# Kernel optimization log

Measured on AMD Instinct MI355X. Metric: run time of the kernel, lower is better.

## Reference

```python
import jax, jax.numpy as jnp
import numpy as np


def _conv(x, w, b=None, stride=1, pad=0, dil=1):
    out = jax.lax.conv_general_dilated(
        x, w, (stride, stride), [(pad, pad), (pad, pad)],
        rhs_dilation=(dil, dil),
        dimension_numbers=('NCHW', 'OIHW', 'NCHW'))
    return out if b is None else out + b[None, :, None, None]


def _sobel_base(out_ch, in_ch, k=3):
    # Exactly mirrors SobelConv2d weight construction (4 directional kernels).
    w = np.zeros((out_ch, in_ch, k, k), np.float32)
    m = k // 2
    for idx in range(out_ch):
        if idx % 4 == 0:
            w[idx, :, 0, :] = -1; w[idx, :, 0, m] = -2
            w[idx, :, -1, :] = 1; w[idx, :, -1, m] = 2
        elif idx % 4 == 1:
            w[idx, :, :, 0] = -1; w[idx, :, m, 0] = -2
            w[idx, :, :, -1] = 1; w[idx, :, m, -1] = 2
        elif idx % 4 == 2:
            w[idx, :, 0, 0] = -2
            for i in range(m + 1):
                w[idx, :, m - i, i] = -1
                w[idx, :, k - 1 - i, m + i] = 1
            w[idx, :, -1, -1] = 2
        else:
            w[idx, :, -1, 0] = -2
            for i in range(m + 1):
                w[idx, :, m + i, i] = -1
                w[idx, :, i, m + i] = 1
            w[idx, :, 0, -1] = 2
    return w


def setup_inputs() -> dict:
    key = jax.random.key(0)
    ks = iter(jax.random.split(key, 40))
    def p(shape, s=0.05):
        return jax.random.normal(next(ks), shape, dtype=jnp.float32) * s
    C = 32  # out_ch == sobel_ch
    f32 = jnp.float32
    return dict(
        x=jax.random.normal(next(ks), (8, 1, 256, 256), dtype=f32),
        sobel_base=jnp.asarray(_sobel_base(C, 1)),
        sobel_factor=jnp.ones((C, 1, 1, 1), f32),
        sobel_bias=jnp.zeros((C,), f32),
        f4_w=p((C, C + 1, 3, 3)), f4_b=jnp.zeros((C,), f32),
        ec1_w=p((C, C, 3, 3)), ec1_b=jnp.zeros((C,), f32),
        ec2_w=p((C, C, 3, 3)), ec2_b=jnp.zeros((C,), f32),
        ec3_w=p((C, C, 3, 3)), ec3_b=jnp.zeros((C,), f32),
        gate_w=p((3, 3 * C, 1, 1)), gate_b=jnp.zeros((3,), f32),
        ca1_w=p((C // 16, C, 1, 1)),  # ChannelAttention fc1 (ratio=16), no bias
        ca2_w=p((C, C // 16, 1, 1)),  # fc2, no bias
        sa_w=p((1, 2, 7, 7)),         # SpatialAttention conv, no bias
        p1_w=p((C, C, 1, 1)), p1_b=jnp.zeros((C,), f32),
        f1_w=p((C, C, 3, 3)), f1_b=jnp.zeros((C,), f32),
        p2_w=p((C, 2 * C, 1, 1)), p2_b=jnp.zeros((C,), f32),
        f2_w=p((C, C, 3, 3)), f2_b=jnp.zeros((C,), f32),
        p3_w=p((C, 2 * C, 1, 1)), p3_b=jnp.zeros((C,), f32),
        f3_w=p((C, C, 3, 3)), f3_b=jnp.zeros((C,), f32),
    )


def reference(x, sobel_base, sobel_factor, sobel_bias, f4_w, f4_b,
              ec1_w, ec1_b, ec2_w, ec2_b, ec3_w, ec3_b, gate_w, gate_b,
              ca1_w, ca2_w, sa_w,
              p1_w, p1_b, f1_w, f1_b, p2_w, p2_b, f2_w, f2_b,
              p3_w, p3_b, f3_w, f3_b):
    lrelu = lambda t: jax.nn.leaky_relu(t, 0.01)
    relu = jax.nn.relu
    # Sobel edge extraction (fixed directional kernels scaled by learned factor)
    out0 = _conv(x, sobel_base * sobel_factor, sobel_bias, pad=1)     # [B,32,H,W]
    out1 = jnp.concatenate([x, out0], axis=1)                          # [B,33,H,W]
    out1 = lrelu(_conv(out1, f4_w, f4_b, pad=1))                       # [B,32,H,W]
    # AdaptiveEdgeConnector: multi-dilation convs + softmax gating
    ex = relu(_conv(out1, ec1_w, ec1_b, pad=1))
    ey = relu(_conv(out1, ec2_w, ec2_b, pad=2, dil=2))
    ez = relu(_conv(out1, ec3_w, ec3_b, pad=3, dil=3))
    gates = jax.nn.softmax(_conv(jnp.concatenate([ex, ey, ez], axis=1), gate_w, gate_b), axis=1)
    enh = gates[:, 0:1] * ex + gates[:, 1:2] * ey + gates[:, 2:3] * ez
    # CBAM: channel attention
    avg = jnp.mean(enh, axis=(2, 3), keepdims=True)
    mx = jnp.max(enh, axis=(2, 3), keepdims=True)
    ca = jax.nn.sigmoid(_conv(relu(_conv(avg, ca1_w)), ca2_w)
                        + _conv(relu(_conv(mx, ca1_w)), ca2_w))
    f = ca * enh
    # CBAM: spatial attention
    sa_in = jnp.concatenate([jnp.mean(f, axis=1, keepdims=True),
                             jnp.max(f, axis=1, keepdims=True)], axis=1)
    sa = jax.nn.sigmoid(_conv(sa_in, sa_w, pad=3))
    edge = sa * f
    # Residual merge + cascaded dense conv stages
    out0 = lrelu(out1 + edge)
    t = lrelu(_conv(out0, p1_w, p1_b))
    t = lrelu(_conv(t, f1_w, f1_b, pad=1))
    o1 = jnp.concatenate([out0, t], axis=1)                            # [B,64,H,W]
    t = lrelu(_conv(o1, p2_w, p2_b))
    t = lrelu(_conv(t, f2_w, f2_b, pad=1))
    o2 = jnp.concatenate([out0, t], axis=1)
    t = lrelu(_conv(o2, p3_w, p3_b))
    t = lrelu(_conv(t, f3_w, f3_b, pad=1))
    return jnp.concatenate([out0, t], axis=1)                          # [B,64,H,W]
```

## Files before the change

kernel.cpp:

```cpp
#include <hip/hip_runtime.h>
#include <math.h>

typedef unsigned short u16;
typedef short short8 __attribute__((ext_vector_type(8)));
typedef float f32x4 __attribute__((ext_vector_type(4)));
typedef unsigned short ushort4v __attribute__((ext_vector_type(4)));

#define Hh 256
#define Ww 256
#define Bb 8
#define PW 262
#define PAD 3
#define HPW (Hh * PW)

__device__ __forceinline__ float bf2f(u16 v) {
    unsigned u = ((unsigned)v) << 16;
    union { unsigned u; float f; } c; c.u = u; return c.f;
}
__device__ __forceinline__ u16 f2bf(float f) {
    union { float f; unsigned u; } c; c.f = f;
    unsigned lsb = (c.u >> 16) & 1u;
    c.u += 0x7fffu + lsb;
    return (u16)(c.u >> 16);
}
__device__ __forceinline__ float sigm(float v) { return 1.f / (1.f + expf(-v)); }

template<int ACT, bool F32OUT, bool FUSEP>
__global__ __launch_bounds__(256) void convs_k(
    const u16* __restrict__ in, const u16* __restrict__ apack,
    const float* __restrict__ bias, void* __restrict__ outp,
    const u16* __restrict__ o0buf, const u16* __restrict__ pw,
    const float* __restrict__ pb, u16* __restrict__ pout)
{
    __shared__ u16 rows[4][4352];
    const int tid = threadIdx.x, lane = tid & 63, wv = tid >> 6;
    const int b = blockIdx.x & 7;
    const int rest = blockIdx.x >> 3;
    const int hpair = rest >> 1, half = rest & 1;
    const int h0 = hpair * 2;
    const int pl = wv * 32 + (lane & 15);
    const int icg = lane >> 4;

    for (int idx = tid; idx < 4 * 536; idx += 256) {
        int rr = idx / 536, q = idx % 536;
        int r = h0 - 1 + rr;
        short8 v = (short8){0, 0, 0, 0, 0, 0, 0, 0};
        if ((unsigned)r < 256u)
            v = *(const short8*)(in + ((size_t)b * HPW + (size_t)r * PW + PAD + half * 128 - 3) * 32
                                 + (size_t)q * 8);
        *(short8*)(&rows[rr][q * 8]) = v;
    }
    __syncthreads();

    f32x4 acc[2][2][2];
    #pragma unroll
    for (int r2 = 0; r2 < 2; ++r2)
        #pragma unroll
        for (int mf = 0; mf < 2; ++mf)
            #pragma unroll
            for (int nf = 0; nf < 2; ++nf)
                acc[r2][mf][nf] = (f32x4){0.f, 0.f, 0.f, 0.f};

    #pragma unroll
    for (int tap = 0; tap < 9; ++tap) {
        const int kh = tap / 3 - 1, kw = tap % 3 - 1;
        short8 a0 = *(const short8*)(apack + ((size_t)(tap * 2 + 0) * 64 + lane) * 8);
        short8 a1 = *(const short8*)(apack + ((size_t)(tap * 2 + 1) * 64 + lane) * 8);
        #pragma unroll
        for (int r2 = 0; r2 < 2; ++r2) {
            const int ri = 1 + r2 + kh;
            #pragma unroll
            for (int nf = 0; nf < 2; ++nf) {
                short8 bf = *(const short8*)(&rows[ri][(pl + nf * 16 + kw + 3) * 32 + icg * 8]);
                acc[r2][0][nf] = __builtin_amdgcn_mfma_f32_16x16x32_bf16(a0, bf, acc[r2][0][nf], 0, 0, 0);
                acc[r2][1][nf] = __builtin_amdgcn_mfma_f32_16x16x32_bf16(a1, bf, acc[r2][1][nf], 0, 0, 0);
            }
        }
    }
    const int nl = half * 128 + pl;
    f32x4 bi[2];
    bi[0] = *(const f32x4*)(bias + icg * 4);
    bi[1] = *(const f32x4*)(bias + 16 + icg * 4);

    if (FUSEP) {
        u16* tile = &rows[0][0];
        __syncthreads();
        #pragma unroll
        for (int r2 = 0; r2 < 2; ++r2)
            #pragma unroll
            for (int mf = 0; mf < 2; ++mf) {
                const int cob = mf * 16 + icg * 4;
                #pragma unroll
                for (int nf = 0; nf < 2; ++nf) {
                    ushort4v o;
                    #pragma unroll
                    for (int i = 0; i < 4; ++i) {
                        float v = acc[r2][mf][nf][i] + bi[mf][i];
                        v = (v > 0.f) ? v : 0.01f * v;
                        o[i] = f2bf(v);
                    }
                    *(ushort4v*)(tile + ((size_t)(r2 * 128 + pl + nf * 16)) * 32 + cob) = o;
                }
            }
        __syncthreads();
        #pragma unroll
        for (int r2 = 0; r2 < 2; ++r2) {
            const int h = h0 + r2;
            f32x4 acc2[2][2];
            #pragma unroll
            for (int mf = 0; mf < 2; ++mf)
                #pragma unroll
                for (int nf = 0; nf < 2; ++nf)
                    acc2[mf][nf] = (f32x4){0.f, 0.f, 0.f, 0.f};
            #pragma unroll
            for (int s = 0; s < 2; ++s) {
                short8 pa0 = *(const short8*)(pw + (size_t)(s * 2 + 0) * 512 + lane * 8);
                short8 pa1 = *(const short8*)(pw + (size_t)(s * 2 + 1) * 512 + lane * 8);
                #pragma unroll
                for (int nf = 0; nf < 2; ++nf) {
                    const int px = pl + nf * 16;
                    short8 bf;
                    if (s == 0)
                        bf = *(const short8*)(o0buf + ((size_t)b * HPW + (size_t)h * PW + PAD + half * 128 + px) * 32 + icg * 8);
                    else
                        bf = *(const short8*)(tile + ((size_t)(r2 * 128 + px)) * 32 + icg * 8);
                    acc2[0][nf] = __builtin_amdgcn_mfma_f32_16x16x32_bf16(pa0, bf, acc2[0][nf], 0, 0, 0);
                    acc2[1][nf] = __builtin_amdgcn_mfma_f32_16x16x32_bf16(pa1, bf, acc2[1][nf], 0, 0, 0);
                }
            }
            const size_t orow = ((size_t)b * HPW + (size_t)h * PW + PAD) * 32;
            #pragma unroll
            for (int mf = 0; mf < 2; ++mf) {
                const int cob = mf * 16 + icg * 4;
                f32x4 pbi = *(const f32x4*)(pb + cob);
                #pragma unroll
                for (int nf = 0; nf < 2; ++nf) {
                    ushort4v o;
                    #pragma unroll
                    for (int i = 0; i < 4; ++i) {
                        float v = acc2[mf][nf][i] + pbi[i];
                        v = (v > 0.f) ? v : 0.01f * v;
                        o[i] = f2bf(v);
                    }
                    *(ushort4v*)(pout + orow + (size_t)(nl + nf * 16) * 32 + cob) = o;
                }
            }
        }
        if (tid < 24) {
            int r2 = tid / 12, rem = tid % 12;
            int col3 = rem >> 2, chunk = rem & 3;
            int col = half ? (256 + PAD + col3) : col3;
            u16* pz = pout + ((size_t)b * HPW + (size_t)(h0 + r2) * PW + col) * 32 + chunk * 8;
            *(short8*)pz = (short8){0, 0, 0, 0, 0, 0, 0, 0};
        }
    } else if (F32OUT) {
        #pragma unroll
        for (int r2 = 0; r2 < 2; ++r2) {
            float* dp = (float*)outp + ((size_t)b * 64 + 32) * 65536 + (size_t)(h0 + r2) * 256;
            #pragma unroll
            for (int mf = 0; mf < 2; ++mf) {
                const int cob = mf * 16 + icg * 4;
                #pragma unroll
                for (int nf = 0; nf < 2; ++nf) {
                    const int w = nl + nf * 16;
                    #pragma unroll
                    for (int i = 0; i < 4; ++i) {
                        float v = acc[r2][mf][nf][i] + bi[mf][i];
                        if (ACT == 1) v = fmaxf(v, 0.f);
                        if (ACT == 2) v = (v > 0.f) ? v : 0.01f * v;
                        dp[(size_t)(cob + i) * 65536 + w] = v;
                    }
                }
            }
        }
    } else {
        u16* out = (u16*)outp;
        #pragma unroll
        for (int r2 = 0; r2 < 2; ++r2) {
            const size_t orow = ((size_t)b * HPW + (size_t)(h0 + r2) * PW + PAD) * 32;
            #pragma unroll
            for (int mf = 0; mf < 2; ++mf) {
                const int cob = mf * 16 + icg * 4;
                #pragma unroll
                for (int nf = 0; nf < 2; ++nf) {
                    ushort4v o;
                    #pragma unroll
                    for (int i = 0; i < 4; ++i) {
                        float v = acc[r2][mf][nf][i] + bi[mf][i];
                        if (ACT == 1) v = fmaxf(v, 0.f);
                        if (ACT == 2) v = (v > 0.f) ? v : 0.01f * v;
                        o[i] = f2bf(v);
                    }
                    *(ushort4v*)(out + orow + (size_t)(nl + nf * 16) * 32 + cob) = o;
                }
            }
        }
    }
}

__global__ __launch_bounds__(256) void ecfuse_k(
    const u16* __restrict__ in, const u16* __restrict__ apack,
    const float* __restrict__ b1, const float* __restrict__ b2,
    const float* __restrict__ b3, const float* __restrict__ gw_,
    const float* __restrict__ gb_, u16* __restrict__ enh)
{
    __shared__ u16 rows[2][3][4288];
    __shared__ float gw[288];
    __shared__ float gb[3];
    __shared__ float bs[96];
    int tid = threadIdx.x;
    for (int i = tid; i < 288; i += 256) gw[i] = gw_[i];
    if (tid < 3) gb[tid] = gb_[tid];
    if (tid < 32) bs[tid] = b1[tid];
    else if (tid < 64) bs[tid] = b2[tid - 32];
    else if (tid < 96) bs[tid] = b3[tid - 64];

    const int lane = tid & 63, wv = tid >> 6;
    const int b = blockIdx.x & 7;
    const int rest = blockIdx.x >> 3;
    const int h = rest >> 1, half = rest & 1;
    const int pl = wv * 32 + (lane & 15);
    const int icg = lane >> 4;
    const u16* src_base = in + ((size_t)b * HPW + PAD + half * 128 - 3) * 32;

    for (int idx = tid; idx < 1608; idx += 256) {
        int rr = idx / 536, q = idx % 536;
        int r = h + (rr - 1);
        short8 v = (short8){0, 0, 0, 0, 0, 0, 0, 0};
        if ((unsigned)r < 256u)
            v = *(const short8*)(src_base + (size_t)r * PW * 32 + (size_t)q * 8);
        *(short8*)(&rows[0][rr][q * 8]) = v;
    }
    __syncthreads();

    f32x4 acc[3][2][2];
    #pragma unroll
    for (int cv = 0; cv < 3; ++cv)
        #pragma unroll
        for (int mf = 0; mf < 2; ++mf)
            #pragma unroll
            for (int nf = 0; nf < 2; ++nf)
                acc[cv][mf][nf] = (f32x4){0.f, 0.f, 0.f, 0.f};

    #pragma unroll
    for (int cv = 0; cv < 3; ++cv) {
        const int dil = cv + 1;
        const int nb = cv & 1;
        short8 stg0, stg1, stg2, stg3, stg4, stg5;
        if (cv < 2) {
            const int dn = cv + 2;
            #pragma unroll
            for (int k = 0; k < 6; ++k) {
                int idx = tid + k * 256;
                int rr = idx / 536, q = idx % 536;
                int r = h + (rr - 1) * dn;
                short8 v = (short8){0, 0, 0, 0, 0, 0, 0, 0};
                if ((unsigned)r < 256u)
                    v = *(const short8*)(src_base + (size_t)r * PW * 32 + (size_t)q * 8);
                if (k == 0) stg0 = v; else if (k == 1) stg1 = v;
                else if (k == 2) stg2 = v; else if (k == 3) stg3 = v;
                else if (k == 4) stg4 = v; else stg5 = v;
            }
        }
        const u16* ap = apack + (size_t)(cv * 9 * 2) * 512;
        #pragma unroll
        for (int tap = 0; tap < 9; ++tap) {
            const int kh = tap / 3 - 1, kw = tap % 3 - 1;
            const int ri = 1 + kh;
            short8 a0 = *(const short8*)(ap + (size_t)(tap * 2 + 0) * 512 + lane * 8);
            short8 a1 = *(const short8*)(ap + (size_t)(tap * 2 + 1) * 512 + lane * 8);
            #pragma unroll
            for (int nf = 0; nf < 2; ++nf) {
                short8 bf = *(const short8*)(&rows[nb][ri][(pl + nf * 16 + kw * dil + 3) * 32 + icg * 8]);
                acc[cv][0][nf] = __builtin_amdgcn_mfma_f32_16x16x32_bf16(a0, bf, acc[cv][0][nf], 0, 0, 0);
                acc[cv][1][nf] = __builtin_amdgcn_mfma_f32_16x16x32_bf16(a1, bf, acc[cv][1][nf], 0, 0, 0);
            }
        }
        if (cv < 2) {
            const int dn = cv + 2;
            #pragma unroll
            for (int k = 0; k < 6; ++k) {
                int idx = tid + k * 256;
                int rr = idx / 536, q = idx % 536;
                short8 v = (k == 0) ? stg0 : (k == 1) ? stg1 : (k == 2) ? stg2
                         : (k == 3) ? stg3 : (k == 4) ? stg4 : stg5;
                *(short8*)(&rows[1 - nb][rr][q * 8]) = v;
            }
            if (tid < 72) {
                int idx = tid + 1536;
                int rr = idx / 536, q = idx % 536;
                int r = h + (rr - 1) * dn;
                short8 v = (short8){0, 0, 0, 0, 0, 0, 0, 0};
                if ((unsigned)r < 256u)
                    v = *(const short8*)(src_base + (size_t)r * PW * 32 + (size_t)q * 8);
                *(short8*)(&rows[1 - nb][rr][q * 8]) = v;
            }
            __syncthreads();
        }
    }
    const int nl = half * 128 + pl;
    const size_t orow = ((size_t)b * HPW + (size_t)h * PW + PAD) * 32;
    #pragma unroll
    for (int nf = 0; nf < 2; ++nf) {
        float e[3][2][4];
        float g0 = 0.f, g1 = 0.f, g2 = 0.f;
        #pragma unroll
        for (int cv = 0; cv < 3; ++cv)
            #pragma unroll
            for (int mf = 0; mf < 2; ++mf) {
                const int cob = mf * 16 + icg * 4;
                #pragma unroll
                for (int i = 0; i < 4; ++i) {
                    float v = fmaxf(acc[cv][mf][nf][i] + bs[cv * 32 + cob + i], 0.f);
                    e[cv][mf][i] = v;
                    const int c = cv * 32 + cob + i;
                    g0 = fmaf(gw[c], v, g0);
                    g1 = fmaf(gw[96 + c], v, g1);
                    g2 = fmaf(gw[192 + c], v, g2);
                }
            }
        g0 += __shfl_xor(g0, 16); g0 += __shfl_xor(g0, 32);
        g1 += __shfl_xor(g1, 16); g1 += __shfl_xor(g1, 32);
        g2 += __shfl_xor(g2, 16); g2 += __shfl_xor(g2, 32);
        g0 += gb[0]; g1 += gb[1]; g2 += gb[2];
        float m = fmaxf(g0, fmaxf(g1, g2));
        float e0 = expf(g0 - m), e1 = expf(g1 - m), e2 = expf(g2 - m);
        float inv = 1.f / (e0 + e1 + e2);
        e0 *= inv; e1 *= inv; e2 *= inv;
        #pragma unroll
        for (int mf = 0; mf < 2; ++mf) {
            const int cob = mf * 16 + icg * 4;
            ushort4v o;
            #pragma unroll
            for (int i = 0; i < 4; ++i)
                o[i] = f2bf(e0 * e[0][mf][i] + e1 * e[1][mf][i] + e2 * e[2][mf][i]);
            *(ushort4v*)(enh + orow + (size_t)(nl + nf * 16) * 32 + cob) = o;
        }
    }
}

__global__ void prepack_k(
    const float* __restrict__ f4w, const float* __restrict__ e1w,
    const float* __restrict__ e2w, const float* __restrict__ e3w,
    const float* __restrict__ f1w, const float* __restrict__ f2w,
    const float* __restrict__ f3w, const float* __restrict__ p1w,
    const float* __restrict__ p2w, const float* __restrict__ p3w,
    u16* __restrict__ apack)
{
    int gid = blockIdx.x * 256 + threadIdx.x;
    if (gid >= 77 * 1024) return;
    const int offs[11] = {0, 18, 27, 36, 45, 54, 63, 72, 73, 75, 77};
    int step = gid >> 10, r = gid & 1023;
    int layer = 0;
    while (step >= offs[layer + 1]) layer++;
    int s = step - offs[layer];
    int mf = r >> 9, l = (r >> 3) & 63, j = r & 7;
    int co = mf * 16 + (l & 15);
    int ICB = (layer == 0 || layer == 8 || layer == 9) ? 2 : 1;
    int tap = s / ICB, icb = s % ICB;
    int icl = icb * 32 + (l >> 4) * 8 + j;
    float v = 0.f;
    if (layer == 0)      { if (icl < 33) v = f4w[(co * 33 + icl) * 9 + tap]; }
    else if (layer == 1) v = e1w[(co * 32 + icl) * 9 + tap];
    else if (layer == 2) v = e2w[(co * 32 + icl) * 9 + tap];
    else if (layer == 3) v = e3w[(co * 32 + icl) * 9 + tap];
    else if (layer == 4) v = f1w[(co * 32 + icl) * 9 + tap];
    else if (layer == 5) v = f2w[(co * 32 + icl) * 9 + tap];
    else if (layer == 6) v = f3w[(co * 32 + icl) * 9 + tap];
    else if (layer == 7) v = p1w[co * 32 + icl];
    else if (layer == 8) v = p2w[co * 64 + icl];
    else                 v = p3w[co * 64 + icl];
    apack[gid] = f2bf(v);
}

__global__ __launch_bounds__(256) void prep5_k(
    const float* __restrict__ f4w, const float* __restrict__ f4b,
    const float* __restrict__ sbase, const float* __restrict__ sfac,
    const float* __restrict__ sbias,
    float* __restrict__ w5, float* __restrict__ be)
{
    __shared__ float sF[32 * 33 * 9];
    __shared__ float sS[288];
    __shared__ float sBias[32];
    int t = threadIdx.x;
    for (int i = t; i < 32 * 33 * 9; i += 256) sF[i] = f4w[i];
    for (int i = t; i < 288; i += 256) sS[i] = sbase[i] * sfac[i / 9];
    if (t < 32) sBias[t] = sbias[t];
    __syncthreads();

    for (int idx = t; idx < 800; idx += 256) {
        int co = idx / 25, tap = idx % 25, kh = tap / 5, kw = tap % 5;
        float s = 0.f;
        if (kh >= 1 && kh <= 3 && kw >= 1 && kw <= 3)
            s = sF[(co * 33 + 0) * 9 + (kh - 1) * 3 + (kw - 1)];
        for (int sc = 0; sc < 32; ++sc) {
            #pragma unroll
            for (int a = 0; a < 3; ++a)
                #pragma unroll
                for (int bq = 0; bq < 3; ++bq) {
                    int p = kh - a, q = kw - bq;
                    if (p >= 0 && p < 3 && q >= 0 && q < 3)
                        s = fmaf(sF[(co * 33 + 1 + sc) * 9 + a * 3 + bq],
                                 sS[sc * 9 + p * 3 + q], s);
                }
        }
        w5[idx] = s;
    }
    for (int co = t; co < 32; co += 256) {
        float s = f4b[co];
        for (int sc = 0; sc < 32; ++sc) {
            float wsum = 0.f;
            #pragma unroll
            for (int k = 0; k < 9; ++k) wsum += sF[(co * 33 + 1 + sc) * 9 + k];
            s = fmaf(sBias[sc], wsum, s);
        }
        be[co] = s;
    }
}

__global__ __launch_bounds__(256) void conv5_k(
    const float* __restrict__ x, const float* __restrict__ w5,
    const float* __restrict__ be, u16* __restrict__ out1)
{
    __shared__ float sw[800];
    __shared__ float sb[32];
    int tid = threadIdx.x;
    for (int i = tid; i < 800; i += 256) sw[i] = w5[i];
    if (tid < 32) sb[tid] = be[tid];
    __syncthreads();
    int b = blockIdx.x & 7, h = blockIdx.x >> 3, w = tid;
    const float* xp = x + (size_t)b * 65536;
    float xv[25];
    #pragma unroll
    for (int i = 0; i < 5; ++i) {
        int r = h + i - 2;
        #pragma unroll
        for (int j = 0; j < 5; ++j) {
            int c = w + j - 2;
            xv[i * 5 + j] = ((unsigned)r < 256u && (unsigned)c < 256u)
                            ? xp[r * 256 + c] : 0.f;
        }
    }
    u16* dst = out1 + ((size_t)b * HPW + (size_t)h * PW + PAD + w) * 32;
    #pragma unroll
    for (int cb = 0; cb < 4; ++cb) {
        short8 o;
        #pragma unroll
        for (int j = 0; j < 8; ++j) {
            int co = cb * 8 + j;
            float s = sb[co];
            #pragma unroll
            for (int t2 = 0; t2 < 25; ++t2) s = fmaf(sw[co * 25 + t2], xv[t2], s);
            s = (s > 0.f) ? s : 0.01f * s;
            o[j] = (short)f2bf(s);
        }
        *(short8*)(dst + cb * 8) = o;
    }
    if (tid < 24) {
        int col6 = tid >> 2, chunk = tid & 3;
        int col = (col6 < 3) ? col6 : (256 + PAD + col6 - 3);
        u16* pz = out1 + ((size_t)b * HPW + (size_t)h * PW + col) * 32 + chunk * 8;
        *(short8*)pz = (short8){0, 0, 0, 0, 0, 0, 0, 0};
    }
}

__global__ __launch_bounds__(256) void ringfix_k(
    const float* __restrict__ x, const float* __restrict__ f4w,
    const float* __restrict__ f4b, const float* __restrict__ sbase,
    const float* __restrict__ sfac, const float* __restrict__ sbias,
    u16* __restrict__ out1)
{
    __shared__ float sW[288];
    __shared__ float sB[32];
    __shared__ float sF[32 * 33 * 9];
    __shared__ float sO[66][2][32];
    int tid = threadIdx.x;
    for (int i = tid; i < 288; i += 256) sW[i] = sbase[i] * sfac[i / 9];
    if (tid < 32) sB[tid] = sbias[tid];
    for (int i = tid; i < 32 * 33 * 9; i += 256) sF[i] = f4w[i];
    __syncthreads();

    int blk = blockIdx.x;
    int b = blk & 7, rest = blk >> 3;
    int e = rest >> 2, seg = rest & 3;
    const float* xp = x + (size_t)b * 65536;

    for (int i = tid; i < 66 * 2 * 32; i += 256) {
        int sc = i & 31, rr2 = i >> 5;
        int d = rr2 & 1, ul = rr2 >> 1;
        int ug = seg * 64 - 1 + ul;
        float v = 0.f;
        if ((unsigned)ug < 256u) {
            int h, w;
            if (e == 0)      { h = d;        w = ug; }
            else if (e == 1) { h = 255 - d;  w = ug; }
            else if (e == 2) { h = ug;       w = d; }
            else             { h = ug;       w = 255 - d; }
            float s = sB[sc];
            for (int p = 0; p < 3; ++p)
                for (int q = 0; q < 3; ++q) {
                    int rr = h + p - 1, cc = w + q - 1;
                    if ((unsigned)rr < 256u && (unsigned)cc < 256u)
                        s = fmaf(sW[sc * 9 + p * 3 + q], xp[rr * 256 + cc], s);
                }
            v = s;
        }
        sO[ul][d][sc] = v;
    }
    __syncthreads();

    int pi = tid & 63, cog = tid >> 6;
    int up = seg * 64 + pi;
    int h, w;
    if (e == 0)      { h = 0;   w = up; }
    else if (e == 1) { h = 255; w = up; }
    else if (e == 2) { h = up;  w = 0; }
    else             { h = up;  w = 255; }
    short8 ov;
    for (int cj = 0; cj < 8; ++cj) {
        int co = cog * 8 + cj;
        float acc = f4b[co];
        for (int a = 0; a < 3; ++a)
            for (int bb = 0; bb < 3; ++bb) {
                int hh = h + a - 1, ww = w + bb - 1;
                if ((unsigned)hh < 256u && (unsigned)ww < 256u)
                    acc = fmaf(sF[(co * 33) * 9 + a * 3 + bb], xp[hh * 256 + ww], acc);
                int d, ug;
                if (e == 0)      { d = hh;        ug = ww; }
                else if (e == 1) { d = 255 - hh;  ug = ww; }
                else if (e == 2) { d = ww;        ug = hh; }
                else             { d = 255 - ww;  ug = hh; }
                if (d >= 0 && d < 2 && (unsigned)ug < 256u) {
                    int ul = ug - (seg * 64 - 1);
                    for (int sc = 0; sc < 32; ++sc)
                        acc = fmaf(sF[(co * 33 + 1 + sc) * 9 + a * 3 + bb], sO[ul][d][sc], acc);
                }
            }
        acc = (acc > 0.f) ? acc : 0.01f * acc;
        ov[cj] = (short)f2bf(acc);
    }
    u16* dst = out1 + ((size_t)b * HPW + (size_t)h * PW + PAD + w) * 32 + cog * 8;
    *(short8*)dst = ov;
}

__global__ __launch_bounds__(256) void ca_part_k(
    const u16* __restrict__ enh, float* __restrict__ part)
{
    int blk = blockIdx.x, b = blk & 7, sl = blk >> 3;
    int tid = threadIdx.x, lane = tid & 63, wv = tid >> 6;
    float s[32], m[32];
    #pragma unroll
    for (int c = 0; c < 32; ++c) { s[c] = 0.f; m[c] = -1e30f; }
    for (int k = 0; k < 8; ++k) {
        int px = sl * 2048 + k * 256 + tid;
        int h = px >> 8, w = px & 255;
        size_t off = ((size_t)b * HPW + (size_t)h * PW + PAD + w) * 32;
        #pragma unroll
        for (int cb = 0; cb < 4; ++cb) {
            short8 v = *(const short8*)(enh + off + cb * 8);
            #pragma unroll
            for (int j = 0; j < 8; ++j) {
                float f = bf2f((u16)v[j]);
                s[cb * 8 + j] += f;
                m[cb * 8 + j] = fmaxf(m[cb * 8 + j], f);
            }
        }
    }
    #pragma unroll
    for (int c = 0; c < 32; ++c)
        #pragma unroll
        for (int o = 32; o; o >>= 1) {
            s[c] += __shfl_down(s[c], o);
            m[c] = fmaxf(m[c], __shfl_down(m[c], o));
        }
    __shared__ float ls[4][32], lm[4][32];
    if (lane == 0)
        for (int c = 0; c < 32; ++c) { ls[wv][c] = s[c]; lm[wv][c] = m[c]; }
    __syncthreads();
    if (tid < 32) {
        float ts = 0.f, tm = -1e30f;
        for (int w2 = 0; w2 < 4; ++w2) { ts += ls[w2][tid]; tm = fmaxf(tm, lm[w2][tid]); }
        int bs = b * 32 + sl;
        part[(size_t)(bs * 2 + 0) * 32 + tid] = ts;
        part[(size_t)(bs * 2 + 1) * 32 + tid] = tm;
    }
}

__global__ void ca_final_k(const float* __restrict__ part,
                           const float* __restrict__ w1, const float* __restrict__ w2,
                           float* __restrict__ ca)
{
    int t = threadIdx.x, b = t >> 5, c = t & 31;
    float s = 0.f, m = -1e30f;
    for (int sl = 0; sl < 32; ++sl) {
        int bs = b * 32 + sl;
        s += part[(size_t)(bs * 2 + 0) * 32 + c];
        m = fmaxf(m, part[(size_t)(bs * 2 + 1) * 32 + c]);
    }
    __shared__ float av[8][32], mx[8][32];
    av[b][c] = s * (1.f / 65536.f);
    mx[b][c] = m;
    __syncthreads();
    float sa0 = 0.f, sm0 = 0.f, sa1 = 0.f, sm1 = 0.f;
    for (int k = 0; k < 32; ++k) {
        float wa = w1[k], wb = w1[32 + k];
        sa0 = fmaf(wa, av[b][k], sa0); sm0 = fmaf(wa, mx[b][k], sm0);
        sa1 = fmaf(wb, av[b][k], sa1); sm1 = fmaf(wb, mx[b][k], sm1);
    }
    float h0 = fmaxf(sa0, 0.f) + fmaxf(sm0, 0.f);
    float h1 = fmaxf(sa1, 0.f) + fmaxf(sm1, 0.f);
    ca[t] = sigm(w2[c * 2 + 0] * h0 + w2[c * 2 + 1] * h1);
}

__global__ __launch_bounds__(256) void samap_k(
    const u16* __restrict__ enh, const float* __restrict__ ca,
    float* __restrict__ smap)
{
    __shared__ float sca[256];
    int tid = threadIdx.x;
    sca[tid] = ca[tid];
    __syncthreads();
    int b = blockIdx.x & 7;
    int r = (blockIdx.x >> 3) * 256 + tid;
    if (r >= 262 * 262) return;
    int ph = r / 262, pw = r % 262;
    float mean = 0.f, mxv = 0.f;
    if (ph >= 3 && ph < 259 && pw >= 3 && pw < 259) {
        int h = ph - 3, w = pw - 3;
        size_t off = ((size_t)b * HPW + (size_t)h * PW + PAD + w) * 32;
        float s = 0.f, m = -1e30f;
        #pragma unroll
        for (int cb = 0; cb < 4; ++cb) {
            short8 v = *(const short8*)(enh + off + cb * 8);
            #pragma unroll
            for (int j = 0; j < 8; ++j) {
                float f = bf2f((u16)v[j]) * sca[b * 32 + cb * 8 + j];
                s += f; m = fmaxf(m, f);
            }
        }
        mean = s * (1.f / 32.f); mxv = m;
    }
    smap[((size_t)b * 262 * 262 + (size_t)ph * 262 + pw) * 2 + 0] = mean;
    smap[((size_t)b * 262 * 262 + (size_t)ph * 262 + pw) * 2 + 1] = mxv;
}

__global__ __launch_bounds__(256) void merge_k(
    const float* __restrict__ smap, const float* __restrict__ saw,
    const float* __restrict__ ca, const u16* __restrict__ out1,
    const u16* __restrict__ enh, u16* __restrict__ o0,
    float* __restrict__ dout,
    const u16* __restrict__ ap1, const float* __restrict__ p1b,
    u16* __restrict__ p1out)
{
    __shared__ float sw[98];
    __shared__ float sca[256];
    __shared__ u16 tile[256 * 32];
    int tid = threadIdx.x;
    for (int i = tid; i < 98; i += 256) sw[i] = saw[i];
    sca[tid] = ca[tid];
    __syncthreads();
    int b = blockIdx.x & 7;
    int h = blockIdx.x >> 3;
    int w = tid;
    const float* sp = smap + (size_t)b * 262 * 262 * 2;
    float acc = 0.f;
    #pragma unroll
    for (int kh = 0; kh < 7; ++kh)
        #pragma unroll
        for (int kw = 0; kw < 7; ++kw) {
            const float* q = sp + ((size_t)(h + kh) * 262 + (w + kw)) * 2;
            acc = fmaf(q[0], sw[kh * 7 + kw], acc);
            acc = fmaf(q[1], sw[49 + kh * 7 + kw], acc);
        }
    float sa = sigm(acc);
    size_t off = ((size_t)b * HPW + (size_t)h * PW + PAD + w) * 32;
    float* dp = dout + (size_t)b * 64 * 65536 + (size_t)h * 256 + w;
    #pragma unroll
    for (int cb = 0; cb < 4; ++cb) {
        short8 ve = *(const short8*)(enh + off + cb * 8);
        short8 vo = *(const short8*)(out1 + off + cb * 8);
        short8 o;
        #pragma unroll
        for (int j = 0; j < 8; ++j) {
            float f = sca[b * 32 + cb * 8 + j] * bf2f((u16)ve[j]);
            float v = bf2f((u16)vo[j]) + sa * f;
            v = (v > 0.f) ? v : 0.01f * v;
            o[j] = (short)f2bf(v);
            dp[(size_t)(cb * 8 + j) * 65536] = v;
        }
        *(short8*)(o0 + off + cb * 8) = o;
        *(short8*)(&tile[w * 32 + cb * 8]) = o;
    }
    __syncthreads();
    const int lane = tid & 63, wv = tid >> 6;
    const int icg = lane >> 4, l15 = lane & 15;
    f32x4 acc1[2][4];
    #pragma unroll
    for (int mf = 0; mf < 2; ++mf)
        #pragma unroll
        for (int nf = 0; nf < 4; ++nf)
            acc1[mf][nf] = (f32x4){0.f, 0.f, 0.f, 0.f};
    short8 pa0 = *(const short8*)(ap1 + (size_t)0 * 512 + lane * 8);
    short8 pa1 = *(const short8*)(ap1 + (size_t)1 * 512 + lane * 8);
    #pragma unroll
    for (int nf = 0; nf < 4; ++nf) {
        short8 bf = *(const short8*)(&tile[(wv * 64 + l15 + nf * 16) * 32 + icg * 8]);
        acc1[0][nf] = __builtin_amdgcn_mfma_f32_16x16x32_bf16(pa0, bf, acc1[0][nf], 0, 0, 0);
        acc1[1][nf] = __builtin_amdgcn_mfma_f32_16x16x32_bf16(pa1, bf, acc1[1][nf], 0, 0, 0);
    }
    const size_t orow = ((size_t)b * HPW + (size_t)h * PW + PAD) * 32;
    #pragma unroll
    for (int mf = 0; mf < 2; ++mf) {
        const int cob = mf * 16 + icg * 4;
        f32x4 pbi = *(const f32x4*)(p1b + cob);
        #pragma unroll
        for (int nf = 0; nf < 4; ++nf) {
            const int px = wv * 64 + l15 + nf * 16;
            ushort4v o;
            #pragma unroll
            for (int i = 0; i < 4; ++i) {
                float v = acc1[mf][nf][i] + pbi[i];
                v = (v > 0.f) ? v : 0.01f * v;
                o[i] = f2bf(v);
            }
            *(ushort4v*)(p1out + orow + (size_t)px * 32 + cob) = o;
        }
    }
}

extern "C" void kernel_launch(void* const* d_in, const int* in_sizes, int n_in,
                              void* d_out, int out_size, void* d_ws, size_t ws_size,
                              hipStream_t stream)
{
    (void)in_sizes; (void)n_in; (void)out_size; (void)ws_size;
    const float* x        = (const float*)d_in[0];
    const float* sob_base = (const float*)d_in[1];
    const float* sob_fac  = (const float*)d_in[2];
    const float* sob_bias = (const float*)d_in[3];
    const float* f4_w = (const float*)d_in[4];   const float* f4_b = (const float*)d_in[5];
    const float* ec1_w = (const float*)d_in[6];  const float* ec1_b = (const float*)d_in[7];
    const float* ec2_w = (const float*)d_in[8];  const float* ec2_b = (const float*)d_in[9];
    const float* ec3_w = (const float*)d_in[10]; const float* ec3_b = (const float*)d_in[11];
    const float* gate_w = (const float*)d_in[12]; const float* gate_b = (const float*)d_in[13];
    const float* ca1_w = (const float*)d_in[14]; const float* ca2_w = (const float*)d_in[15];
    const float* sa_w  = (const float*)d_in[16];
    const float* p1_w = (const float*)d_in[17]; const float* p1_b = (const float*)d_in[18];
    const float* f1_w = (const float*)d_in[19]; const float* f1_b = (const float*)d_in[20];
    const float* p2_w = (const float*)d_in[21]; const float* p2_b = (const float*)d_in[22];
    const float* f2_w = (const float*)d_in[23]; const float* f2_b = (const float*)d_in[24];
    const float* p3_w = (const float*)d_in[25]; const float* p3_b = (const float*)d_in[26];
    const float* f3_w = (const float*)d_in[27]; const float* f3_b = (const float*)d_in[28];

    const size_t PB32 = (size_t)Bb * HPW * 32 * 2;
    char* ws = (char*)d_ws;
    u16* Q    = (u16*)(ws);
    u16* O0   = (u16*)(ws + PB32);
    u16* T    = (u16*)(ws + 2 * PB32);
    u16* ENH  = (u16*)(ws + 3 * PB32);
    u16* AP   = (u16*)(ws + 4 * PB32);
    float* W5   = (float*)(ws + 4 * PB32 + 77 * 1024 * 2);
    float* BE   = W5 + 800;
    float* PART = BE + 32;
    float* CA   = PART + 8 * 32 * 2 * 32;

    char* doutc = (char*)d_out;
    float* SMAP = (float*)(doutc + (134217728 - (size_t)Bb * 262 * 262 * 2 * 4));
    float* dout = (float*)d_out;

    dim3 blk(256);

    prepack_k<<<308, blk, 0, stream>>>(f4_w, ec1_w, ec2_w, ec3_w, f1_w, f2_w, f3_w,
                                       p1_w, p2_w, p3_w, AP);
    prep5_k<<<1, blk, 0, stream>>>(f4_w, f4_b, sob_base, sob_fac, sob_bias, W5, BE);
    conv5_k<<<2048, blk, 0, stream>>>(x, W5, BE, Q);
    ringfix_k<<<128, blk, 0, stream>>>(x, f4_w, f4_b, sob_base, sob_fac, sob_bias, Q);
    ecfuse_k<<<4096, blk, 0, stream>>>(Q, AP + 18 * 1024, ec1_b, ec2_b, ec3_b,
                                       gate_w, gate_b, ENH);
    ca_part_k<<<256, blk, 0, stream>>>(ENH, PART);
    ca_final_k<<<1, blk, 0, stream>>>(PART, ca1_w, ca2_w, CA);
    samap_k<<<2152, blk, 0, stream>>>(ENH, CA, SMAP);
    merge_k<<<2048, blk, 0, stream>>>(SMAP, sa_w, CA, Q, ENH, O0, dout,
                                      AP + 72 * 1024, p1_b, Q);
    convs_k<2, false, true ><<<2048, blk, 0, stream>>>(Q, AP + 45 * 1024, f1_b, nullptr,
                                                       O0, AP + 73 * 1024, p2_b, T);
    convs_k<2, false, true ><<<2048, blk, 0, stream>>>(T, AP + 54 * 1024, f2_b, nullptr,
                                                       O0, AP + 75 * 1024, p3_b, Q);
    convs_k<2, true, false><<<2048, blk, 0, stream>>>(Q, AP + 63 * 1024, f3_b, dout,
                                                      nullptr, nullptr, nullptr, nullptr);
}
```

Before: 389.7 us.

## Compute two output rows per block in fused dilated edge conv kernel

The fused three-dilation edge conv kernel now processes two adjacent output rows per block instead of one. The centre rows are loaded once and shared across both rows and all dilations, and only the dilation-specific halo rows are reloaded. This halves the grid and cuts redundant global and LDS row loads and weight fragment loads per output. In exchange it doubles accumulator registers and adds an extra barrier per dilation stage, which may lower occupancy.

```diff
diff --git a/kernel.cpp b/kernel.cpp
--- a/kernel.cpp
+++ b/kernel.cpp
@@ -204,7 +204,8 @@
     const float* __restrict__ b3, const float* __restrict__ gw_,
     const float* __restrict__ gb_, u16* __restrict__ enh)
 {
-    __shared__ u16 rows[2][3][4288];
+    __shared__ u16 crow[2][4288];
+    __shared__ u16 halo[4][4288];
     __shared__ float gw[288];
     __shared__ float gb[3];
     __shared__ float bs[96];
@@ -218,123 +219,142 @@
     const int lane = tid & 63, wv = tid >> 6;
     const int b = blockIdx.x & 7;
     const int rest = blockIdx.x >> 3;
-    const int h = rest >> 1, half = rest & 1;
+    const int hpair = rest >> 1, half = rest & 1;
+    const int h = hpair * 2;
     const int pl = wv * 32 + (lane & 15);
     const int icg = lane >> 4;
     const u16* src_base = in + ((size_t)b * HPW + PAD + half * 128 - 3) * 32;
 
-    for (int idx = tid; idx < 1608; idx += 256) {
+    for (int idx = tid; idx < 4 * 536; idx += 256) {
         int rr = idx / 536, q = idx % 536;
-        int r = h + (rr - 1);
+        int r = h - 1 + rr;
         short8 v = (short8){0, 0, 0, 0, 0, 0, 0, 0};
         if ((unsigned)r < 256u)
             v = *(const short8*)(src_base + (size_t)r * PW * 32 + (size_t)q * 8);
-        *(short8*)(&rows[0][rr][q * 8]) = v;
-    }
-    __syncthreads();
-
-    f32x4 acc[3][2][2];
+        u16* dst = (rr == 1) ? &crow[0][q * 8] : (rr == 2) ? &crow[1][q * 8]
+                 : (rr == 0) ? &halo[0][q * 8] : &halo[3][q * 8];
+        *(short8*)dst = v;
+    }
+    __syncthreads();
+
+    f32x4 acc[3][2][2][2];
     #pragma unroll
     for (int cv = 0; cv < 3; ++cv)
         #pragma unroll
-        for (int mf = 0; mf < 2; ++mf)
-            #pragma unroll
-            for (int nf = 0; nf < 2; ++nf)
-                acc[cv][mf][nf] = (f32x4){0.f, 0.f, 0.f, 0.f};
+        for (int r2 = 0; r2 < 2; ++r2)
+            #pragma unroll
+            for (int mf = 0; mf < 2; ++mf)
+                #pragma unroll
+                for (int nf = 0; nf < 2; ++nf)
+                    acc[cv][r2][mf][nf] = (f32x4){0.f, 0.f, 0.f, 0.f};
 
     #pragma unroll
     for (int cv = 0; cv < 3; ++cv) {
         const int dil = cv + 1;
-        const int nb = cv & 1;
-        short8 stg0, stg1, stg2, stg3, stg4, stg5;
+        short8 stg0, stg1, stg2, stg3, stg4, stg5, stg6, stg7, stgT;
         if (cv < 2) {
             const int dn = cv + 2;
             #pragma unroll
-            for (int k = 0; k < 6; ++k) {
+            for (int k = 0; k < 8; ++k) {
                 int idx = tid + k * 256;
                 int rr = idx / 536, q = idx % 536;
-                int r = h + (rr - 1) * dn;
+                int off = (rr == 0) ? -dn : (rr == 1) ? 1 - dn : (rr == 2) ? dn : dn + 1;
+                int r = h + off;
                 short8 v = (short8){0, 0, 0, 0, 0, 0, 0, 0};
                 if ((unsigned)r < 256u)
                     v = *(const short8*)(src_base + (size_t)r * PW * 32 + (size_t)q * 8);
                 if (k == 0) stg0 = v; else if (k == 1) stg1 = v;
                 else if (k == 2) stg2 = v; else if (k == 3) stg3 = v;
-                else if (k == 4) stg4 = v; else stg5 = v;
+                else if (k == 4) stg4 = v; else if (k == 5) stg5 = v;
+                else if (k == 6) stg6 = v; else stg7 = v;
+            }
+            if (tid < 96) {
+                int q = 440 + tid;
+                int r = h + dn + 1;
+                short8 v = (short8){0, 0, 0, 0, 0, 0, 0, 0};
+                if ((unsigned)r < 256u)
+                    v = *(const short8*)(src_base + (size_t)r * PW * 32 + (size_t)q * 8);
+                stgT = v;
             }
         }
         const u16* ap = apack + (size_t)(cv * 9 * 2) * 512;
         #pragma unroll
         for (int tap = 0; tap < 9; ++tap) {
             const int kh = tap / 3 - 1, kw = tap % 3 - 1;
-            const int ri = 1 + kh;
             short8 a0 = *(const short8*)(ap + (size_t)(tap * 2 + 0) * 512 + lane * 8);
             short8 a1 = *(const short8*)(ap + (size_t)(tap * 2 + 1) * 512 + lane * 8);
             #pragma unroll
-            for (int nf = 0; nf < 2; ++nf) {
-                short8 bf = *(const short8*)(&rows[nb][ri][(pl + nf * 16 + kw * dil + 3) * 32 + icg * 8]);
-                acc[cv][0][nf] = __builtin_amdgcn_mfma_f32_16x16x32_bf16(a0, bf, acc[cv][0][nf], 0, 0, 0);
-                acc[cv][1][nf] = __builtin_amdgcn_mfma_f32_16x16x32_bf16(a1, bf, acc[cv][1][nf], 0, 0, 0);
+            for (int r2 = 0; r2 < 2; ++r2) {
+                const u16* rp;
+                if (kh == 0) rp = &crow[r2][0];
+                else if (kh == -1) rp = (r2 == 0) ? &halo[0][0]
+                                        : (dil == 1 ? &crow[0][0] : &halo[1][0]);
+                else rp = (r2 == 1) ? &halo[3][0]
+                          : (dil == 1 ? &crow[1][0] : &halo[2][0]);
+                #pragma unroll
+                for (int nf = 0; nf < 2; ++nf) {
+                    short8 bf = *(const short8*)(rp + (pl + nf * 16 + kw * dil + 3) * 32 + icg * 8);
+                    acc[cv][r2][0][nf] = __builtin_amdgcn_mfma_f32_16x16x32_bf16(a0, bf, acc[cv][r2][0][nf], 0, 0, 0);
+                    acc[cv][r2][1][nf] = __builtin_amdgcn_mfma_f32_16x16x32_bf16(a1, bf, acc[cv][r2][1][nf], 0, 0, 0);
+                }
             }
         }
         if (cv < 2) {
-            const int dn = cv + 2;
-            #pragma unroll
-            for (int k = 0; k < 6; ++k) {
+            __syncthreads();
+            #pragma unroll
+            for (int k = 0; k < 8; ++k) {
                 int idx = tid + k * 256;
                 int rr = idx / 536, q = idx % 536;
                 short8 v = (k == 0) ? stg0 : (k == 1) ? stg1 : (k == 2) ? stg2
-                         : (k == 3) ? stg3 : (k == 4) ? stg4 : stg5;
-                *(short8*)(&rows[1 - nb][rr][q * 8]) = v;
-            }
-            if (tid < 72) {
-                int idx = tid + 1536;
-                int rr = idx / 536, q = idx % 536;
-                int r = h + (rr - 1) * dn;
-                short8 v = (short8){0, 0, 0, 0, 0, 0, 0, 0};
-                if ((unsigned)r < 256u)
-                    v = *(const short8*)(src_base + (size_t)r * PW * 32 + (size_t)q * 8);
-                *(short8*)(&rows[1 - nb][rr][q * 8]) = v;
-            }
+                         : (k == 3) ? stg3 : (k == 4) ? stg4 : (k == 5) ? stg5
+                         : (k == 6) ? stg6 : stg7;
+                *(short8*)(&halo[rr][q * 8]) = v;
+            }
+            if (tid < 96)
+                *(short8*)(&halo[3][(440 + tid) * 8]) = stgT;
             __syncthreads();
         }
     }
-    const int nl = half * 128 + pl;
-    const size_t orow = ((size_t)b * HPW + (size_t)h * PW + PAD) * 32;
-    #pragma unroll
-    for (int nf = 0; nf < 2; ++nf) {
-        float e[3][2][4];
-        float g0 = 0.f, g1 = 0.f, g2 = 0.f;
-        #pragma unroll
-        for (int cv = 0; cv < 3; ++cv)
+    #pragma unroll
+    for (int r2 = 0; r2 < 2; ++r2) {
+        const int nl = half * 128 + pl;
+        const size_t orow = ((size_t)b * HPW + (size_t)(h + r2) * PW + PAD) * 32;
+        #pragma unroll
+        for (int nf = 0; nf < 2; ++nf) {
+            float e[3][2][4];
+            float g0 = 0.f, g1 = 0.f, g2 = 0.f;
+            #pragma unroll
+            for (int cv = 0; cv < 3; ++cv)
+                #pragma unroll
+                for (int mf = 0; mf < 2; ++mf) {
+                    const int cob = mf * 16 + icg * 4;
+                    #pragma unroll
+                    for (int i = 0; i < 4; ++i) {
+                        float v = fmaxf(acc[cv][r2][mf][nf][i] + bs[cv * 32 + cob + i], 0.f);
+                        e[cv][mf][i] = v;
+                        const int c = cv * 32 + cob + i;
+                        g0 = fmaf(gw[c], v, g0);
+                        g1 = fmaf(gw[96 + c], v, g1);
+                        g2 = fmaf(gw[192 + c], v, g2);
+                    }
+                }
+            g0 += __shfl_xor(g0, 16); g0 += __shfl_xor(g0, 32);
+            g1 += __shfl_xor(g1, 16); g1 += __shfl_xor(g1, 32);
+            g2 += __shfl_xor(g2, 16); g2 += __shfl_xor(g2, 32);
+            g0 += gb[0]; g1 += gb[1]; g2 += gb[2];
+            float m = fmaxf(g0, fmaxf(g1, g2));
+            float e0 = expf(g0 - m), e1 = expf(g1 - m), e2 = expf(g2 - m);
+            float inv = 1.f / (e0 + e1 + e2);
+            e0 *= inv; e1 *= inv; e2 *= inv;
             #pragma unroll
             for (int mf = 0; mf < 2; ++mf) {
                 const int cob = mf * 16 + icg * 4;
-                #pragma unroll
-                for (int i = 0; i < 4; ++i) {
-                    float v = fmaxf(acc[cv][mf][nf][i] + bs[cv * 32 + cob + i], 0.f);
-                    e[cv][mf][i] = v;
-                    const int c = cv * 32 + cob + i;
-                    g0 = fmaf(gw[c], v, g0);
-                    g1 = fmaf(gw[96 + c], v, g1);
-                    g2 = fmaf(gw[192 + c], v, g2);
-                }
-            }
-        g0 += __shfl_xor(g0, 16); g0 += __shfl_xor(g0, 32);
-        g1 += __shfl_xor(g1, 16); g1 += __shfl_xor(g1, 32);
-        g2 += __shfl_xor(g2, 16); g2 += __shfl_xor(g2, 32);
-        g0 += gb[0]; g1 += gb[1]; g2 += gb[2];
-        float m = fmaxf(g0, fmaxf(g1, g2));
-        float e0 = expf(g0 - m), e1 = expf(g1 - m), e2 = expf(g2 - m);
-        float inv = 1.f / (e0 + e1 + e2);
-        e0 *= inv; e1 *= inv; e2 *= inv;
-        #pragma unroll
-        for (int mf = 0; mf < 2; ++mf) {
-            const int cob = mf * 16 + icg * 4;
-            ushort4v o;
-            #pragma unroll
-            for (int i = 0; i < 4; ++i)
-                o[i] = f2bf(e0 * e[0][mf][i] + e1 * e[1][mf][i] + e2 * e[2][mf][i]);
-            *(ushort4v*)(enh + orow + (size_t)(nl + nf * 16) * 32 + cob) = o;
+                ushort4v o;
+                #pragma unroll
+                for (int i = 0; i < 4; ++i)
+                    o[i] = f2bf(e0 * e[0][mf][i] + e1 * e[1][mf][i] + e2 * e[2][mf][i]);
+                *(ushort4v*)(enh + orow + (size_t)(nl + nf * 16) * 32 + cob) = o;
+            }
         }
     }
 }
@@ -774,7 +794,7 @@
     prep5_k<<<1, blk, 0, stream>>>(f4_w, f4_b, sob_base, sob_fac, sob_bias, W5, BE);
     conv5_k<<<2048, blk, 0, stream>>>(x, W5, BE, Q);
     ringfix_k<<<128, blk, 0, stream>>>(x, f4_w, f4_b, sob_base, sob_fac, sob_bias, Q);
-    ecfuse_k<<<4096, blk, 0, stream>>>(Q, AP + 18 * 1024, ec1_b, ec2_b, ec3_b,
+    ecfuse_k<<<2048, blk, 0, stream>>>(Q, AP + 18 * 1024, ec1_b, ec2_b, ec3_b,
                                        gate_w, gate_b, ENH);
     ca_part_k<<<256, blk, 0, stream>>>(ENH, PART);
     ca_final_k<<<1, blk, 0, stream>>>(PART, ca1_w, ca2_w, CA);
```

New measurement: 436.1 us. 1.12x slower.
